# Performance work log

Hardware: AMD Instinct MI355X
Metric: run time of the kernel (lower is better)

Reference implementation:

```python
import jax, jax.numpy as jnp
import numpy as np

N = 50000
NEG_SLOPE = 0.2  # PyG GATConv default negative_slope


def gat_conv(x, src, dst, W, a_src, a_dst, b, heads, out_dim, concat):
    # x: [N, F_in]; W: [F_in, heads*out_dim]; a_src/a_dst: [heads, out_dim]
    h = (x @ W).reshape(N, heads, out_dim)                      # [N,H,D]
    alpha_src = jnp.einsum('nhd,hd->nh', h, a_src)              # [N,H]
    alpha_dst = jnp.einsum('nhd,hd->nh', h, a_dst)              # [N,H]
    e = jax.nn.leaky_relu(alpha_src[src] + alpha_dst[dst], NEG_SLOPE)  # [E,H]
    # segment softmax over incoming edges of each destination node
    m = jax.ops.segment_max(e, dst, num_segments=N)             # [N,H]
    ex = jnp.exp(e - m[dst])
    denom = jax.ops.segment_sum(ex, dst, num_segments=N)        # [N,H]
    alpha = ex / (denom[dst] + 1e-16)                           # [E,H]
    msg = h[src] * alpha[:, :, None]                            # [E,H,D]
    out = jax.ops.segment_sum(msg, dst, num_segments=N)         # [N,H,D]
    out = out.reshape(N, heads * out_dim) if concat else out.mean(axis=1)
    return out + b


def setup_inputs() -> dict:
    key = jax.random.key(0)
    ks = jax.random.split(key, 14)
    E = 800000
    IN, HID, H, LAT = 128, 64, 4, 64

    def glorot(k, shape):
        fan = shape[0] + shape[-1]
        return jax.random.uniform(k, shape, jnp.float32, -1.0, 1.0) * np.sqrt(6.0 / fan)

    return {
        'x': jax.random.normal(ks[0], (N, IN), jnp.float32),
        'edge_index': jax.random.randint(ks[1], (2, E), 0, N, jnp.int64),
        'W1': glorot(ks[2], (IN, H * HID)),
        'a_src1': glorot(ks[3], (H, HID)),
        'a_dst1': glorot(ks[4], (H, HID)),
        'b1': jnp.zeros((H * HID,), jnp.float32),
        'W_mu': glorot(ks[5], (H * HID, LAT)),
        'a_src_mu': glorot(ks[6], (1, LAT)),
        'a_dst_mu': glorot(ks[7], (1, LAT)),
        'b_mu': jnp.zeros((LAT,), jnp.float32),
        'W_ls': glorot(ks[8], (H * HID, LAT)),
        'a_src_ls': glorot(ks[9], (1, LAT)),
        'a_dst_ls': glorot(ks[10], (1, LAT)),
        'b_ls': jnp.zeros((LAT,), jnp.float32),
    }


def reference(x, edge_index, W1, a_src1, a_dst1, b1,
              W_mu, a_src_mu, a_dst_mu, b_mu,
              W_ls, a_src_ls, a_dst_ls, b_ls):
    # PyG GATConv adds self-loops by default
    loops = jnp.arange(N, dtype=edge_index.dtype)
    src = jnp.concatenate([edge_index[0], loops])
    dst = jnp.concatenate([edge_index[1], loops])

    h = jax.nn.relu(gat_conv(x, src, dst, W1, a_src1, a_dst1, b1, 4, 64, True))
    mu = gat_conv(h, src, dst, W_mu, a_src_mu, a_dst_mu, b_mu, 1, 64, False)
    logstd = gat_conv(h, src, dst, W_ls, a_src_ls, a_dst_ls, b_ls, 1, 64, False)
    return (mu, logstd)
```

## Files before the change

### kernel.cpp

```cpp
#include <hip/hip_runtime.h>
#include <hip/hip_bf16.h>

#define NNODES 50000
#define MT 3125
#define NB 196
typedef __hip_bfloat16 bf16;
typedef __attribute__((ext_vector_type(8))) short bf16x8;
typedef __attribute__((ext_vector_type(4))) float f32x4;

__device__ __forceinline__ void unpack2(unsigned w, float& lo, float& hi){
  lo = __uint_as_float(w << 16);
  hi = __uint_as_float(w & 0xffff0000u);
}
__device__ __forceinline__ short f2bf(float f){
  union { __hip_bfloat16 h; short s; } u; u.h = __float2bfloat16(f); return u.s;
}
__device__ __forceinline__ float lrelu(float v){ return v > 0.f ? v : 0.2f * v; }

__global__ __launch_bounds__(256)
void cvt_w_k(const float* __restrict__ W1, const float* __restrict__ Wmu,
             const float* __restrict__ Wls, bf16x8* __restrict__ Bp1,
             bf16x8* __restrict__ Bp2){
  int t = blockIdx.x * 256 + threadIdx.x;
  if (t < 4096){
    int lane = t & 63, ct = (t >> 6) & 15, kt = t >> 10;
    int k0 = kt * 32 + (lane >> 4) * 8, col = ct * 16 + (lane & 15);
    bf16x8 o;
    #pragma unroll
    for (int j = 0; j < 8; j++) o[j] = f2bf(W1[(size_t)(k0 + j) * 256 + col]);
    Bp1[t] = o;
  } else if (t < 8192){
    int u = t - 4096;
    int lane = u & 63, ct = (u >> 6) & 7, kt = u >> 9;
    int k0 = kt * 32 + (lane >> 4) * 8, col = ct * 16 + (lane & 15);
    const float* W = (col < 64) ? Wmu : Wls;
    int cc = col & 63;
    bf16x8 o;
    #pragma unroll
    for (int j = 0; j < 8; j++) o[j] = f2bf(W[(size_t)(k0 + j) * 64 + cc]);
    Bp2[u] = o;
  }
}

__global__ __launch_bounds__(256)
void gemm1_mfma(const float* __restrict__ x, const bf16x8* __restrict__ Bp,
                const float* __restrict__ aS, const float* __restrict__ aD,
                bf16* __restrict__ Y, float* __restrict__ as1, float* __restrict__ ad1){
  int rt = blockIdx.x;
  int w = threadIdx.x >> 6, lane = threadIdx.x & 63;
  const float* xr = x + (size_t)(rt * 16 + (lane & 15)) * 128 + (lane >> 4) * 8;
  f32x4 z = {0.f, 0.f, 0.f, 0.f};
  f32x4 acc[4] = {z, z, z, z};
  for (int kt = 0; kt < 4; kt++){
    float4 v0 = *(const float4*)(xr + kt * 32);
    float4 v1 = *(const float4*)(xr + kt * 32 + 4);
    bf16x8 a;
    a[0] = f2bf(v0.x); a[1] = f2bf(v0.y); a[2] = f2bf(v0.z); a[3] = f2bf(v0.w);
    a[4] = f2bf(v1.x); a[5] = f2bf(v1.y); a[6] = f2bf(v1.z); a[7] = f2bf(v1.w);
    #pragma unroll
    for (int c = 0; c < 4; c++){
      bf16x8 b = Bp[(size_t)(kt * 16 + w * 4 + c) * 64 + lane];
      acc[c] = __builtin_amdgcn_mfma_f32_16x16x32_bf16(a, b, acc[c], 0, 0, 0);
    }
  }
  int row0 = rt * 16 + (lane >> 4) * 4;
  #pragma unroll
  for (int c = 0; c < 4; c++){
    int col = w * 64 + c * 16 + (lane & 15);
    #pragma unroll
    for (int i = 0; i < 4; i++)
      Y[(size_t)(row0 + i) * 256 + col] = __float2bfloat16(acc[c][i]);
  }
  float aSv[4], aDv[4];
  #pragma unroll
  for (int c = 0; c < 4; c++){
    int col = c * 16 + (lane & 15);
    aSv[c] = aS[w * 64 + col];
    aDv[c] = aD[w * 64 + col];
  }
  #pragma unroll
  for (int i = 0; i < 4; i++){
    float s1 = 0.f, s2 = 0.f;
    #pragma unroll
    for (int c = 0; c < 4; c++){
      s1 = fmaf(acc[c][i], aSv[c], s1);
      s2 = fmaf(acc[c][i], aDv[c], s2);
    }
    #pragma unroll
    for (int o = 1; o < 16; o <<= 1){
      s1 += __shfl_xor(s1, o);
      s2 += __shfl_xor(s2, o);
    }
    if ((lane & 15) == 0){
      int node = row0 + i;
      as1[node * 4 + w] = s1;
      ad1[node * 4 + w] = s2;
    }
  }
}

__global__ __launch_bounds__(256)
void gemm2_mfma(const bf16x8* __restrict__ Ap, const bf16x8* __restrict__ Bp,
                const float* __restrict__ aSmu, const float* __restrict__ aDmu,
                const float* __restrict__ aSls, const float* __restrict__ aDls,
                bf16* __restrict__ Y2,
                float* __restrict__ as2m, float* __restrict__ ad2m,
                float* __restrict__ as2l, float* __restrict__ ad2l){
  int w = threadIdx.x >> 6, lane = threadIdx.x & 63;
  int rt = blockIdx.x * 4 + w;
  if (rt >= MT) return;
  f32x4 z = {0.f, 0.f, 0.f, 0.f};
  f32x4 acc[8] = {z, z, z, z, z, z, z, z};
  for (int kt = 0; kt < 8; kt++){
    bf16x8 a = Ap[(size_t)(rt * 8 + kt) * 64 + lane];
    #pragma unroll
    for (int c = 0; c < 8; c++){
      bf16x8 b = Bp[(size_t)(kt * 8 + c) * 64 + lane];
      acc[c] = __builtin_amdgcn_mfma_f32_16x16x32_bf16(a, b, acc[c], 0, 0, 0);
    }
  }
  int row0 = rt * 16 + (lane >> 4) * 4;
  #pragma unroll
  for (int c = 0; c < 4; c++){
    int col = c * 16 + (lane & 15);
    #pragma unroll
    for (int i = 0; i < 4; i++){
      Y2[(size_t)(row0 + i) * 128 + col]       = __float2bfloat16(acc[c][i]);
      Y2[(size_t)(row0 + i) * 128 + 64 + col]  = __float2bfloat16(acc[4 + c][i]);
    }
  }
  float aSm[4], aDm[4], aSl[4], aDl[4];
  #pragma unroll
  for (int c = 0; c < 4; c++){
    int col = c * 16 + (lane & 15);
    aSm[c] = aSmu[col]; aDm[c] = aDmu[col];
    aSl[c] = aSls[col]; aDl[c] = aDls[col];
  }
  #pragma unroll
  for (int i = 0; i < 4; i++){
    float s1 = 0.f, s2 = 0.f, s3 = 0.f, s4 = 0.f;
    #pragma unroll
    for (int c = 0; c < 4; c++){
      s1 = fmaf(acc[c][i], aSm[c], s1);
      s2 = fmaf(acc[c][i], aDm[c], s2);
      s3 = fmaf(acc[4 + c][i], aSl[c], s3);
      s4 = fmaf(acc[4 + c][i], aDl[c], s4);
    }
    #pragma unroll
    for (int o = 1; o < 16; o <<= 1){
      s1 += __shfl_xor(s1, o);
      s2 += __shfl_xor(s2, o);
      s3 += __shfl_xor(s3, o);
      s4 += __shfl_xor(s4, o);
    }
    if ((lane & 15) == 0){
      int node = row0 + i;
      as2m[node] = s1; ad2m[node] = s2;
      as2l[node] = s3; ad2l[node] = s4;
    }
  }
}

__global__ __launch_bounds__(256)
void bhist_k(const int* __restrict__ ei, int E0, int Etot, int* __restrict__ bcnt){
  __shared__ int lh[NB];
  for (int i = threadIdx.x; i < NB; i += 256) lh[i] = 0;
  __syncthreads();
  int base = blockIdx.x * 1024 + threadIdx.x;
  #pragma unroll
  for (int q = 0; q < 4; q++){
    int e = base + q * 256;
    if (e < Etot){
      int d = (e < E0) ? ei[E0 + e] : e - E0;
      atomicAdd(&lh[d >> 8], 1);
    }
  }
  __syncthreads();
  for (int i = threadIdx.x; i < NB; i += 256)
    if (lh[i]) atomicAdd(&bcnt[i], lh[i]);
}

__global__ __launch_bounds__(256)
void bscan_k(const int* __restrict__ bcnt, int* __restrict__ bbase,
             int* __restrict__ bcur, int total){
  __shared__ int buf[256];
  int t = threadIdx.x;
  int v = (t < NB) ? bcnt[t] : 0;
  buf[t] = v; __syncthreads();
  int acc = v;
  for (int off = 1; off < 256; off <<= 1){
    int x = (t >= off) ? buf[t - off] : 0;
    __syncthreads();
    acc += x; buf[t] = acc; __syncthreads();
  }
  if (t < NB){ int ex = acc - v; bbase[t] = ex; bcur[t] = ex; }
  if (t == 0) bbase[NB] = total;
}

__global__ __launch_bounds__(256)
void bscat_k(const int* __restrict__ ei, int E0, int Etot,
             int* __restrict__ bcur, unsigned* __restrict__ buck){
  __shared__ int lh[NB];
  __shared__ int lbase[NB];
  for (int i = threadIdx.x; i < NB; i += 256) lh[i] = 0;
  __syncthreads();
  int base = blockIdx.x * 1024 + threadIdx.x;
  int sA[4], dA[4], rA[4];
  #pragma unroll
  for (int q = 0; q < 4; q++){
    int e = base + q * 256;
    sA[q] = -1;
    if (e < Etot){
      int s, d;
      if (e < E0){ s = ei[e]; d = ei[E0 + e]; } else { s = d = e - E0; }
      sA[q] = s; dA[q] = d;
      rA[q] = atomicAdd(&lh[d >> 8], 1);
    }
  }
  __syncthreads();
  for (int i = threadIdx.x; i < NB; i += 256)
    lbase[i] = lh[i] ? atomicAdd(&bcur[i], lh[i]) : 0;
  __syncthreads();
  #pragma unroll
  for (int q = 0; q < 4; q++){
    if (sA[q] >= 0){
      int bk = dA[q] >> 8;
      buck[lbase[bk] + rA[q]] = ((unsigned)(dA[q] & 255) << 16) | (unsigned)sA[q];
    }
  }
}

__global__ __launch_bounds__(256)
void bcsr_k(const unsigned* __restrict__ buck, const int* __restrict__ bbase,
            int* __restrict__ offs, int* __restrict__ srcs, int n){
  int b = blockIdx.x;
  int lo = bbase[b], hi = bbase[b + 1];
  __shared__ int eh[256];
  __shared__ int buf[256];
  int t = threadIdx.x;
  eh[t] = 0;
  __syncthreads();
  for (int j = lo + t; j < hi; j += 256)
    atomicAdd(&eh[(buck[j] >> 16) & 255], 1);
  __syncthreads();
  int v = eh[t];
  buf[t] = v; __syncthreads();
  int acc = v;
  for (int off = 1; off < 256; off <<= 1){
    int x = (t >= off) ? buf[t - off] : 0;
    __syncthreads();
    acc += x; buf[t] = acc; __syncthreads();
  }
  int loff = acc - v;
  int node = b * 256 + t;
  if (node < n) offs[node] = lo + loff;
  if (b == NB - 1 && t == 0) offs[n] = bbase[NB];
  __syncthreads();
  eh[t] = loff;
  __syncthreads();
  for (int j = lo + t; j < hi; j += 256){
    unsigned val = buck[j];
    int dlo = (val >> 16) & 255;
    int rank = atomicAdd(&eh[dlo], 1);
    srcs[lo + rank] = (int)(val & 0xffffu);
  }
}

__global__ __launch_bounds__(128)
void gat_aggr1_k(const int* __restrict__ offs, const int* __restrict__ srcs,
                 const float* __restrict__ as, const float* __restrict__ ad,
                 const bf16* __restrict__ h, const float* __restrict__ b,
                 bf16x8* __restrict__ Ap2, int n){
  int node = blockIdx.x * 2 + (threadIdx.x >> 6);
  if (node >= n) return;
  int lane = threadIdx.x & 63;
  int beg = offs[node], end = offs[node + 1];
  int hA = lane >> 4, iA = lane & 15;
  float advA = ad[node * 4 + hA];
  float m = -1e30f;
  for (int j = beg + iA; j < end; j += 16)
    m = fmaxf(m, lrelu(as[srcs[j] * 4 + hA] + advA));
  #pragma unroll
  for (int o = 1; o < 16; o <<= 1) m = fmaxf(m, __shfl_xor(m, o));
  int hP = (lane >> 3) & 3, oct = lane & 7, slot = lane >> 5;
  float mP   = __shfl(m, hP * 16);
  float advP = __shfl(advA, hP * 16);
  float s = 0.f;
  float acc[8];
  #pragma unroll
  for (int i = 0; i < 8; i++) acc[i] = 0.f;
  #pragma unroll 8
  for (int j0 = beg; j0 < end; j0 += 2){
    int j = j0 + slot;
    if (j < end){
      int si = srcs[j];
      float e = lrelu(as[si * 4 + hP] + advP);
      float p = __expf(e - mP);
      s += p;
      uint4 dw = *(const uint4*)(h + (size_t)si * 256 + hP * 64 + oct * 8);
      float lo, hi;
      unpack2(dw.x, lo, hi); acc[0] = fmaf(lo, p, acc[0]); acc[1] = fmaf(hi, p, acc[1]);
      unpack2(dw.y, lo, hi); acc[2] = fmaf(lo, p, acc[2]); acc[3] = fmaf(hi, p, acc[3]);
      unpack2(dw.z, lo, hi); acc[4] = fmaf(lo, p, acc[4]); acc[5] = fmaf(hi, p, acc[5]);
      unpack2(dw.w, lo, hi); acc[6] = fmaf(lo, p, acc[6]); acc[7] = fmaf(hi, p, acc[7]);
    }
  }
  s += __shfl_xor(s, 32);
  #pragma unroll
  for (int i = 0; i < 8; i++) acc[i] += __shfl_xor(acc[i], 32);
  if (lane < 32){
    float inv = 1.f / (s + 1e-16f);
    bf16x8 o;
    #pragma unroll
    for (int i = 0; i < 8; i++){
      float vv = acc[i] * inv + b[lane * 8 + i];
      o[i] = f2bf(vv > 0.f ? vv : 0.f);
    }
    int kt = lane >> 2, g = lane & 3;
    int rt = node >> 4, r = node & 15;
    Ap2[(size_t)(rt * 8 + kt) * 64 + g * 16 + r] = o;
  }
}

__global__ __launch_bounds__(128)
void gat_aggr2_k(const int* __restrict__ offs, const int* __restrict__ srcs,
                 const float* __restrict__ as2m, const float* __restrict__ ad2m,
                 const float* __restrict__ as2l, const float* __restrict__ ad2l,
                 const bf16* __restrict__ h2,
                 const float* __restrict__ bmu, const float* __restrict__ bls,
                 float* __restrict__ outmu, float* __restrict__ outls, int n){
  int node = blockIdx.x * 2 + (threadIdx.x >> 6);
  if (node >= n) return;
  int lane = threadIdx.x & 63;
  int beg = offs[node], end = offs[node + 1];
  const float* asA = (lane >= 32) ? as2l : as2m;
  float advA = ((lane >= 32) ? ad2l : ad2m)[node];
  int iA = lane & 31;
  float m = -1e30f;
  for (int j = beg + iA; j < end; j += 32)
    m = fmaxf(m, lrelu(asA[srcs[j]] + advA));
  #pragma unroll
  for (int o = 1; o < 32; o <<= 1) m = fmaxf(m, __shfl_xor(m, o));
  int br = (lane >> 3) & 1, oct = lane & 7, slot = lane >> 4;
  float mP   = __shfl(m, br * 32);
  float advP = __shfl(advA, br * 32);
  const float* asP = br ? as2l : as2m;
  float s = 0.f;
  float acc[8];
  #pragma unroll
  for (int i = 0; i < 8; i++) acc[i] = 0.f;
  #pragma unroll 4
  for (int j0 = beg; j0 < end; j0 += 4){
    int j = j0 + slot;
    if (j < end){
      int si = srcs[j];
      float e = lrelu(asP[si] + advP);
      float p = __expf(e - mP);
      s += p;
      uint4 dw = *(const uint4*)(h2 + (size_t)si * 128 + br * 64 + oct * 8);
      float lo, hi;
      unpack2(dw.x, lo, hi); acc[0] = fmaf(lo, p, acc[0]); acc[1] = fmaf(hi, p, acc[1]);
      unpack2(dw.y, lo, hi); acc[2] = fmaf(lo, p, acc[2]); acc[3] = fmaf(hi, p, acc[3]);
      unpack2(dw.z, lo, hi); acc[4] = fmaf(lo, p, acc[4]); acc[5] = fmaf(hi, p, acc[5]);
      unpack2(dw.w, lo, hi); acc[6] = fmaf(lo, p, acc[6]); acc[7] = fmaf(hi, p, acc[7]);
    }
  }
  #pragma unroll
  for (int off = 16; off <= 32; off <<= 1){
    s += __shfl_xor(s, off);
    #pragma unroll
    for (int i = 0; i < 8; i++) acc[i] += __shfl_xor(acc[i], off);
  }
  if (lane < 16){
    float inv = 1.f / (s + 1e-16f);
    const float* bb = (lane >= 8) ? bls : bmu;
    float* out = (lane >= 8) ? outls : outmu;
    float v[8];
    #pragma unroll
    for (int i = 0; i < 8; i++) v[i] = acc[i] * inv + bb[oct * 8 + i];
    float* op = out + (size_t)node * 64 + oct * 8;
    *(float4*)op       = make_float4(v[0], v[1], v[2], v[3]);
    *(float4*)(op + 4) = make_float4(v[4], v[5], v[6], v[7]);
  }
}

extern "C" void kernel_launch(void* const* d_in, const int* in_sizes, int n_in,
                              void* d_out, int out_size, void* d_ws, size_t ws_size,
                              hipStream_t stream){
  const float* x    = (const float*)d_in[0];
  const int*   ei   = (const int*)d_in[1];
  const float* W1   = (const float*)d_in[2];
  const float* aS1  = (const float*)d_in[3];
  const float* aD1  = (const float*)d_in[4];
  const float* b1   = (const float*)d_in[5];
  const float* Wmu  = (const float*)d_in[6];
  const float* aSmu = (const float*)d_in[7];
  const float* aDmu = (const float*)d_in[8];
  const float* bmu  = (const float*)d_in[9];
  const float* Wls  = (const float*)d_in[10];
  const float* aSls = (const float*)d_in[11];
  const float* aDls = (const float*)d_in[12];
  const float* bls  = (const float*)d_in[13];

  const int N    = NNODES;
  const int E0   = in_sizes[1] / 2;
  const int Etot = E0 + N;

  float* ws = (float*)d_ws;
  bf16x8* Ap2  = (bf16x8*)(ws);
  bf16*   h1bf = (bf16*)(ws + 6400000);
  bf16*   h2   = (bf16*)(ws + 12800000);
  float*  as1  = ws + 16000000;
  float*  ad1  = ws + 16200000;
  float*  as2m = ws + 16400000;
  float*  ad2m = ws + 16450000;
  float*  as2l = ws + 16500000;
  float*  ad2l = ws + 16550000;
  int*      offs  = (int*)(ws + 16600000);
  int*      srcs  = (int*)(ws + 16650016);
  unsigned* buck  = (unsigned*)(ws + 17500016);
  int*      bcnt  = (int*)(ws + 18350016);
  int*      bbase = (int*)(ws + 18350272);
  int*      bcur  = (int*)(ws + 18350544);
  bf16x8*   Bp1   = (bf16x8*)(ws + 18351040);
  bf16x8*   Bp2   = (bf16x8*)(ws + 18367424);

  float* outmu = (float*)d_out;
  float* outls = (float*)d_out + 3200000;

  const int egrid4 = (Etot + 1023) / 1024;

  hipMemsetAsync(bcnt, 0, 256 * sizeof(int), stream);
  bhist_k<<<egrid4, 256, 0, stream>>>(ei, E0, Etot, bcnt);
  bscan_k<<<1, 256, 0, stream>>>(bcnt, bbase, bcur, Etot);
  bscat_k<<<egrid4, 256, 0, stream>>>(ei, E0, Etot, bcur, buck);
  bcsr_k<<<NB, 256, 0, stream>>>(buck, bbase, offs, srcs, N);

  cvt_w_k<<<32, 256, 0, stream>>>(W1, Wmu, Wls, Bp1, Bp2);

  gemm1_mfma<<<MT, 256, 0, stream>>>(x, Bp1, aS1, aD1, h1bf, as1, ad1);
  gat_aggr1_k<<<(N + 1) / 2, 128, 0, stream>>>(offs, srcs, as1, ad1, h1bf, b1, Ap2, N);

  gemm2_mfma<<<(MT + 3) / 4, 256, 0, stream>>>(Ap2, Bp2, aSmu, aDmu, aSls, aDls,
                                               h2, as2m, ad2m, as2l, ad2l);
  gat_aggr2_k<<<(N + 1) / 2, 128, 0, stream>>>(offs, srcs, as2m, ad2m, as2l, ad2l,
                                               h2, bmu, bls, outmu, outls, N);
}
```

Before: 232.1 us.

## Replace per-node segment max with global upper-bound shift for softmax

Drops the per-destination max pass over incoming edges in both aggregation kernels. Instead, small reduction kernels compute the global max of source attention logits per head, and each node uses lrelu(global_max + ad[node]) as the softmax shift. Leaky ReLU is monotonic, so this value bounds every incoming edge score and the normalised result is mathematically the same. This removes a full gather pass over srcs and the attention-score arrays, but adds two small kernels and a memset, and can underflow exp when a node's edge scores sit far below the bound.

Measured after the change: 247.1 us. 1.06x slower.

```diff
diff --git a/kernel.cpp b/kernel.cpp
--- a/kernel.cpp
+++ b/kernel.cpp
@@ -16,6 +16,14 @@
   union { __hip_bfloat16 h; short s; } u; u.h = __float2bfloat16(f); return u.s;
 }
 __device__ __forceinline__ float lrelu(float v){ return v > 0.f ? v : 0.2f * v; }
+__device__ __forceinline__ unsigned fenc(float f){
+  unsigned u = __float_as_uint(f);
+  return (u & 0x80000000u) ? ~u : (u | 0x80000000u);
+}
+__device__ __forceinline__ float fdec(unsigned u){
+  unsigned b = (u & 0x80000000u) ? (u & 0x7fffffffu) : ~u;
+  return __uint_as_float(b);
+}
 
 __global__ __launch_bounds__(256)
 void cvt_w_k(const float* __restrict__ W1, const float* __restrict__ Wmu,
@@ -162,6 +170,48 @@
 }
 
 __global__ __launch_bounds__(256)
+void gmax1_k(const float* __restrict__ as1, unsigned* __restrict__ gm, int n){
+  float4 mx = make_float4(-1e30f, -1e30f, -1e30f, -1e30f);
+  for (int i = blockIdx.x * 256 + threadIdx.x; i < n; i += gridDim.x * 256){
+    float4 v = *(const float4*)(as1 + (size_t)i * 4);
+    mx.x = fmaxf(mx.x, v.x); mx.y = fmaxf(mx.y, v.y);
+    mx.z = fmaxf(mx.z, v.z); mx.w = fmaxf(mx.w, v.w);
+  }
+  #pragma unroll
+  for (int o = 1; o < 64; o <<= 1){
+    mx.x = fmaxf(mx.x, __shfl_xor(mx.x, o));
+    mx.y = fmaxf(mx.y, __shfl_xor(mx.y, o));
+    mx.z = fmaxf(mx.z, __shfl_xor(mx.z, o));
+    mx.w = fmaxf(mx.w, __shfl_xor(mx.w, o));
+  }
+  if ((threadIdx.x & 63) == 0){
+    atomicMax(&gm[0], fenc(mx.x));
+    atomicMax(&gm[1], fenc(mx.y));
+    atomicMax(&gm[2], fenc(mx.z));
+    atomicMax(&gm[3], fenc(mx.w));
+  }
+}
+
+__global__ __launch_bounds__(256)
+void gmax2_k(const float* __restrict__ asm_, const float* __restrict__ asl,
+             unsigned* __restrict__ gm, int n){
+  float m1 = -1e30f, m2 = -1e30f;
+  for (int i = blockIdx.x * 256 + threadIdx.x; i < n; i += gridDim.x * 256){
+    m1 = fmaxf(m1, asm_[i]);
+    m2 = fmaxf(m2, asl[i]);
+  }
+  #pragma unroll
+  for (int o = 1; o < 64; o <<= 1){
+    m1 = fmaxf(m1, __shfl_xor(m1, o));
+    m2 = fmaxf(m2, __shfl_xor(m2, o));
+  }
+  if ((threadIdx.x & 63) == 0){
+    atomicMax(&gm[4], fenc(m1));
+    atomicMax(&gm[5], fenc(m2));
+  }
+}
+
+__global__ __launch_bounds__(256)
 void bhist_k(const int* __restrict__ ei, int E0, int Etot, int* __restrict__ bcnt){
   __shared__ int lh[NB];
   for (int i = threadIdx.x; i < NB; i += 256) lh[i] = 0;
@@ -269,22 +319,16 @@
 __global__ __launch_bounds__(128)
 void gat_aggr1_k(const int* __restrict__ offs, const int* __restrict__ srcs,
                  const float* __restrict__ as, const float* __restrict__ ad,
+                 const unsigned* __restrict__ gm,
                  const bf16* __restrict__ h, const float* __restrict__ b,
                  bf16x8* __restrict__ Ap2, int n){
   int node = blockIdx.x * 2 + (threadIdx.x >> 6);
   if (node >= n) return;
   int lane = threadIdx.x & 63;
   int beg = offs[node], end = offs[node + 1];
-  int hA = lane >> 4, iA = lane & 15;
-  float advA = ad[node * 4 + hA];
-  float m = -1e30f;
-  for (int j = beg + iA; j < end; j += 16)
-    m = fmaxf(m, lrelu(as[srcs[j] * 4 + hA] + advA));
-  #pragma unroll
-  for (int o = 1; o < 16; o <<= 1) m = fmaxf(m, __shfl_xor(m, o));
   int hP = (lane >> 3) & 3, oct = lane & 7, slot = lane >> 5;
-  float mP   = __shfl(m, hP * 16);
-  float advP = __shfl(advA, hP * 16);
+  float advP = ad[node * 4 + hP];
+  float mP = lrelu(fdec(gm[hP]) + advP);
   float s = 0.f;
   float acc[8];
   #pragma unroll
@@ -326,6 +370,7 @@
 void gat_aggr2_k(const int* __restrict__ offs, const int* __restrict__ srcs,
                  const float* __restrict__ as2m, const float* __restrict__ ad2m,
                  const float* __restrict__ as2l, const float* __restrict__ ad2l,
+                 const unsigned* __restrict__ gm,
                  const bf16* __restrict__ h2,
                  const float* __restrict__ bmu, const float* __restrict__ bls,
                  float* __restrict__ outmu, float* __restrict__ outls, int n){
@@ -333,18 +378,10 @@
   if (node >= n) return;
   int lane = threadIdx.x & 63;
   int beg = offs[node], end = offs[node + 1];
-  const float* asA = (lane >= 32) ? as2l : as2m;
-  float advA = ((lane >= 32) ? ad2l : ad2m)[node];
-  int iA = lane & 31;
-  float m = -1e30f;
-  for (int j = beg + iA; j < end; j += 32)
-    m = fmaxf(m, lrelu(asA[srcs[j]] + advA));
-  #pragma unroll
-  for (int o = 1; o < 32; o <<= 1) m = fmaxf(m, __shfl_xor(m, o));
   int br = (lane >> 3) & 1, oct = lane & 7, slot = lane >> 4;
-  float mP   = __shfl(m, br * 32);
-  float advP = __shfl(advA, br * 32);
   const float* asP = br ? as2l : as2m;
+  float advP = (br ? ad2l : ad2m)[node];
+  float mP = lrelu(fdec(gm[4 + br]) + advP);
   float s = 0.f;
   float acc[8];
   #pragma unroll
@@ -422,6 +459,7 @@
   int*      bcnt  = (int*)(ws + 18350016);
   int*      bbase = (int*)(ws + 18350272);
   int*      bcur  = (int*)(ws + 18350544);
+  unsigned* gm    = (unsigned*)(ws + 18350800);
   bf16x8*   Bp1   = (bf16x8*)(ws + 18351040);
   bf16x8*   Bp2   = (bf16x8*)(ws + 18367424);
 
@@ -431,6 +469,7 @@
   const int egrid4 = (Etot + 1023) / 1024;
 
   hipMemsetAsync(bcnt, 0, 256 * sizeof(int), stream);
+  hipMemsetAsync(gm, 0, 8 * sizeof(unsigned), stream);
   bhist_k<<<egrid4, 256, 0, stream>>>(ei, E0, Etot, bcnt);
   bscan_k<<<1, 256, 0, stream>>>(bcnt, bbase, bcur, Etot);
   bscat_k<<<egrid4, 256, 0, stream>>>(ei, E0, Etot, bcur, buck);
@@ -439,10 +478,12 @@
   cvt_w_k<<<32, 256, 0, stream>>>(W1, Wmu, Wls, Bp1, Bp2);
 
   gemm1_mfma<<<MT, 256, 0, stream>>>(x, Bp1, aS1, aD1, h1bf, as1, ad1);
-  gat_aggr1_k<<<(N + 1) / 2, 128, 0, stream>>>(offs, srcs, as1, ad1, h1bf, b1, Ap2, N);
+  gmax1_k<<<64, 256, 0, stream>>>(as1, gm, N);
+  gat_aggr1_k<<<(N + 1) / 2, 128, 0, stream>>>(offs, srcs, as1, ad1, gm, h1bf, b1, Ap2, N);
 
   gemm2_mfma<<<(MT + 3) / 4, 256, 0, stream>>>(Ap2, Bp2, aSmu, aDmu, aSls, aDls,
                                                h2, as2m, ad2m, as2l, ad2l);
+  gmax2_k<<<64, 256, 0, stream>>>(as2m, as2l, gm, N);
   gat_aggr2_k<<<(N + 1) / 2, 128, 0, stream>>>(offs, srcs, as2m, ad2m, as2l, ad2l,
-                                               h2, bmu, bls, outmu, outls, N);
-}
+                                               gm, h2, bmu, bls, outmu, outls, N);
+}
```
